# Performance work log

Measured on AMD Instinct MI355X. Metric: run time of the kernel, lower is better.

## Reference

```python
import jax, jax.numpy as jnp
import numpy as np

ALPHA = 0.2          # LeakyReLU negative slope
NEG_INF = -9e15      # mask value from the original code


def setup_inputs() -> dict:
    key = jax.random.key(0)
    k1, k2, k3, k4 = jax.random.split(key, 4)
    B, N, F_in, F_out = 8, 2048, 64, 64
    x = jax.random.normal(k1, (B, N, F_in), dtype=jnp.float32)
    adj = jax.random.randint(k2, (B, N, N), 0, 2, dtype=jnp.int32)
    W = jax.random.normal(k3, (F_in, F_out), dtype=jnp.float32)
    a = jax.random.normal(k4, (2 * F_out, 1), dtype=jnp.float32)
    return {"x": x, "adj": adj, "W": W, "a": a}


def reference(x, adj, W, a):
    # h: [B, N, F_out]
    h = jnp.matmul(x, W)
    F_out = W.shape[1]
    a1 = a[:F_out, 0]   # source half of attention vector
    a2 = a[F_out:, 0]   # target half
    # e_ij = leakyrelu(h_i . a1 + h_j . a2)  -- identical math to the
    # original cat([h_i, h_j]) @ a without materializing [B,N*N,2F].
    s1 = jnp.einsum('bnf,f->bn', h, a1)  # [B, N]
    s2 = jnp.einsum('bnf,f->bn', h, a2)  # [B, N]
    e = jax.nn.leaky_relu(s1[:, :, None] + s2[:, None, :], negative_slope=ALPHA)
    masked = jnp.where(adj > 0, e, NEG_INF)
    attention = jax.nn.softmax(masked, axis=2)  # [B, N, N]
    # dropout p=0.0 / eval mode -> identity
    h_prime = jnp.matmul(attention, h)          # [B, N, F_out]
    return jax.nn.elu(h_prime)                  # concat=True branch
```

## Files before the change

### kernel.cpp

```cpp
#include <hip/hip_runtime.h>
#include <cstdint>

#define LRELU_ALPHA 0.2f
#define NEG_INF -9000000000000000.0f
#define L2E 1.4426950408889634f

typedef __bf16 bf16x8 __attribute__((ext_vector_type(8)));
typedef float floatx4 __attribute__((ext_vector_type(4)));
typedef unsigned int uintx4 __attribute__((ext_vector_type(4)));

constexpr int Bb = 8, Nn = 2048, Ff = 64;
constexpr int TJ = 64;
constexpr int SEGW = 8;
constexpr int SLICE = Nn / SEGW;
constexpr int NT = SLICE / TJ;
constexpr int NROWS = Bb * Nn;
constexpr int MCH = Nn / 64;

__device__ __forceinline__ unsigned short f2bf(float f) {
    unsigned u = __builtin_bit_cast(unsigned, f);
    u = u + 0x7FFFu + ((u >> 16) & 1u);
    return (unsigned short)(u >> 16);
}

__device__ __forceinline__ unsigned cvt_pk_bf16(float lo, float hi) {
    unsigned r;
    asm("v_cvt_pk_bf16_f32 %0, %1, %2" : "=v"(r) : "v"(lo), "v"(hi));
    return r;
}

__global__ __launch_bounds__(256) void gat_prep(
    const float* __restrict__ x, const float* __restrict__ W, const float* __restrict__ a,
    unsigned short* __restrict__ hT, float* __restrict__ s1g, float* __restrict__ s2g)
{
    constexpr int STR2 = 36;
    __shared__ unsigned short hblk[64 * STR2];
    const int tid = threadIdx.x;
    const int blk = blockIdx.x;
    const int b  = blk >> 6;
    const int i0 = (blk & 63) * 32;
    const int w    = tid >> 6;
    const int lane = tid & 63;

    float wcol[64];
    #pragma unroll
    for (int k = 0; k < 64; ++k) wcol[k] = W[k * 64 + lane];
    const float a1 = a[lane], a2 = a[64 + lane];

    for (int r = 0; r < 8; ++r) {
        const int il = w * 8 + r;
        const int i  = i0 + il;
        const float* xrow = x + ((size_t)(b * Nn + i)) * 64;
        float h0 = 0.f, h1 = 0.f, h2 = 0.f, h3 = 0.f;
        #pragma unroll
        for (int k = 0; k < 64; k += 4) {
            h0 = fmaf(xrow[k],     wcol[k],     h0);
            h1 = fmaf(xrow[k + 1], wcol[k + 1], h1);
            h2 = fmaf(xrow[k + 2], wcol[k + 2], h2);
            h3 = fmaf(xrow[k + 3], wcol[k + 3], h3);
        }
        const float h = (h0 + h1) + (h2 + h3);
        float p1 = h * a1, p2 = h * a2;
        #pragma unroll
        for (int off = 32; off; off >>= 1) {
            p1 += __shfl_xor(p1, off);
            p2 += __shfl_xor(p2, off);
        }
        if (lane == 0) { s1g[b * Nn + i] = p1; s2g[b * Nn + i] = p2; }
        hblk[lane * STR2 + il] = f2bf(h);
    }
    __syncthreads();
    {
        const int f = tid >> 2, c = (tid & 3) * 8;
        uint4 v = *reinterpret_cast<const uint4*>(&hblk[f * STR2 + c]);
        *reinterpret_cast<uint4*>(hT + ((size_t)b * 64 + f) * Nn + i0 + c) = v;
    }
}

__global__ __launch_bounds__(256) void gat_pack(
    const int* __restrict__ adj, const float* __restrict__ s1g, const float* __restrict__ s2g,
    unsigned long long* __restrict__ masks, float* __restrict__ row_m)
{
    const int wid  = blockIdx.x * 4 + (threadIdx.x >> 6);
    const int lane = threadIdx.x & 63;
    #pragma unroll
    for (int rr = 0; rr < 2; ++rr) {
        const int row = wid * 2 + rr;
        const int b   = row >> 11;
        const int* ar = adj + (size_t)row * Nn;
        const float* s2r = s2g + (size_t)b * Nn;
        unsigned long long acc = 0;
        float mx = NEG_INF;
        #pragma unroll
        for (int cb = 0; cb < MCH; ++cb) {
            const int   v  = ar[cb * 64 + lane];
            const float sv = s2r[cb * 64 + lane];
            const unsigned long long mb = __ballot(v > 0);
            if (lane == cb) acc = mb;
            mx = (v > 0) ? fmaxf(mx, sv) : mx;
        }
        #pragma unroll
        for (int off = 32; off; off >>= 1) mx = fmaxf(mx, __shfl_xor(mx, off));
        if (lane < 32) masks[(size_t)row * MCH + lane] = acc;
        if (lane == 0) {
            const float ev = s1g[row] + mx;
            row_m[row] = fmaxf(ev, LRELU_ALPHA * ev);
        }
    }
}

__global__ __launch_bounds__(512, 4) void gat_attn(
    const unsigned long long* __restrict__ masks, const unsigned short* __restrict__ hT,
    const float* __restrict__ s1g, const float* __restrict__ s2g,
    const float* __restrict__ row_m, float* __restrict__ out)
{
    __shared__ float O_lds[SEGW][16][65];
    __shared__ float l_lds[SEGW][16];

    const int tid  = threadIdx.x;
    const int blk  = blockIdx.x;
    const int b    = blk >> 7;
    const int i0   = (blk & 127) * 16;
    const int s    = tid >> 6;
    const int lane = tid & 63;
    const int fl   = lane & 15;
    const int q    = lane >> 4;

    const int i = i0 + fl;
    const float s1v = s1g[b * Nn + i];
    const float ci  = -row_m[b * Nn + i] * L2E;
    const unsigned short* hTb = hT + (size_t)b * 64 * Nn + s * SLICE;
    const float* s2b = s2g + b * Nn + s * SLICE;
    const unsigned long long* mrow = masks + (size_t)(b * Nn + i) * MCH + s * NT;

    float l = 0.f;
    floatx4 C[4] = {};

    #pragma unroll
    for (int jt = 0; jt < NT; ++jt) {
        const int jloc = jt * TJ;

        const unsigned long long mk = mrow[jt];
        const float4 sA = *reinterpret_cast<const float4*>(&s2b[jloc + q * 8]);
        const float4 sB = *reinterpret_cast<const float4*>(&s2b[jloc + q * 8 + 4]);
        const float4 sC = *reinterpret_cast<const float4*>(&s2b[jloc + 32 + q * 8]);
        const float4 sD = *reinterpret_cast<const float4*>(&s2b[jloc + 32 + q * 8 + 4]);

        bf16x8 Bv[8];
        #pragma unroll
        for (int u = 0; u < 4; ++u) {
            Bv[2 * u] = *reinterpret_cast<const bf16x8*>(
                hTb + (size_t)(u * 16 + fl) * Nn + jloc + q * 8);
            Bv[2 * u + 1] = *reinterpret_cast<const bf16x8*>(
                hTb + (size_t)(u * 16 + fl) * Nn + jloc + 32 + q * 8);
        }

        const unsigned blo = ((unsigned)(mk >> (q * 8))) & 0xFFu;
        const unsigned bhi = ((unsigned)(mk >> (32 + q * 8))) & 0xFFu;

        float p[16];
        {
            const float s2v0[8] = { sA.x, sA.y, sA.z, sA.w, sB.x, sB.y, sB.z, sB.w };
            const float s2v1[8] = { sC.x, sC.y, sC.z, sC.w, sD.x, sD.y, sD.z, sD.w };
            #pragma unroll
            for (int jj = 0; jj < 8; ++jj) {
                float ev = s1v + s2v0[jj];
                ev = fmaxf(ev, LRELU_ALPHA * ev);
                const float t = exp2f(fmaf(ev, L2E, ci));
                p[jj] = (blo & (1u << jj)) ? t : 0.f;
                l += p[jj];
            }
            #pragma unroll
            for (int jj = 0; jj < 8; ++jj) {
                float ev = s1v + s2v1[jj];
                ev = fmaxf(ev, LRELU_ALPHA * ev);
                const float t = exp2f(fmaf(ev, L2E, ci));
                p[8 + jj] = (bhi & (1u << jj)) ? t : 0.f;
                l += p[8 + jj];
            }
        }

        uintx4 pa, pb;
        #pragma unroll
        for (int d = 0; d < 4; ++d) {
            pa[d] = cvt_pk_bf16(p[2 * d],     p[2 * d + 1]);
            pb[d] = cvt_pk_bf16(p[8 + 2 * d], p[8 + 2 * d + 1]);
        }
        const bf16x8 A0 = __builtin_bit_cast(bf16x8, pa);
        const bf16x8 A1 = __builtin_bit_cast(bf16x8, pb);

        __builtin_amdgcn_s_setprio(1);
        #pragma unroll
        for (int u = 0; u < 4; ++u) {
            C[u] = __builtin_amdgcn_mfma_f32_16x16x32_bf16(A0, Bv[2 * u],     C[u], 0, 0, 0);
            C[u] = __builtin_amdgcn_mfma_f32_16x16x32_bf16(A1, Bv[2 * u + 1], C[u], 0, 0, 0);
        }
        __builtin_amdgcn_s_setprio(0);
    }

    l += __shfl_xor(l, 16);
    l += __shfl_xor(l, 32);

    #pragma unroll
    for (int u = 0; u < 4; ++u)
        #pragma unroll
        for (int r = 0; r < 4; ++r)
            O_lds[s][q * 4 + r][u * 16 + fl] = C[u][r];
    if (q == 0) l_lds[s][fl] = l;
    __syncthreads();

    const int row = tid >> 5;
    const int f0  = (tid & 31) * 2;

    float lsum = 0.f, acc0 = 0.f, acc1 = 0.f;
    #pragma unroll
    for (int k = 0; k < SEGW; ++k) {
        lsum += l_lds[k][row];
        const float2 ov = *reinterpret_cast<const float2*>(&O_lds[k][row][f0]);
        acc0 += ov.x;
        acc1 += ov.y;
    }
    const float inv = 1.f / lsum;
    float v0 = acc0 * inv, v1 = acc1 * inv;
    v0 = (v0 > 0.f) ? v0 : (exp2f(v0 * L2E) - 1.f);
    v1 = (v1 > 0.f) ? v1 : (exp2f(v1 * L2E) - 1.f);
    float2 o2; o2.x = v0; o2.y = v1;
    *reinterpret_cast<float2*>(&out[((size_t)(b * Nn + i0 + row)) * 64 + f0]) = o2;
}

extern "C" void kernel_launch(void* const* d_in, const int* in_sizes, int n_in,
                              void* d_out, int out_size, void* d_ws, size_t ws_size,
                              hipStream_t stream) {
    const float* x   = (const float*)d_in[0];
    const int*   adj = (const int*)d_in[1];
    const float* W   = (const float*)d_in[2];
    const float* a   = (const float*)d_in[3];
    float* out = (float*)d_out;

    char* p = (char*)d_ws;
    unsigned short* hT = (unsigned short*)p;  p += (size_t)Bb * 64 * Nn * sizeof(unsigned short);
    float* s1 = (float*)p;                    p += (size_t)NROWS * sizeof(float);
    float* s2 = (float*)p;                    p += (size_t)NROWS * sizeof(float);
    unsigned long long* masks = (unsigned long long*)p;
    p += (size_t)NROWS * MCH * sizeof(unsigned long long);
    float* row_m = (float*)p;

    gat_prep<<<dim3(Bb * Nn / 32), dim3(256), 0, stream>>>(x, W, a, hT, s1, s2);
    gat_pack<<<dim3(NROWS / 8), dim3(256), 0, stream>>>(adj, s1, s2, masks, row_m);
    gat_attn<<<dim3(NROWS / 16), dim3(512), 0, stream>>>(masks, hT, s1, s2, row_m, out);
}
```

Before: 271.4 us.

## Fuse adjacency bit-packing into attention kernel and use per-batch max bound

```diff
diff --git a/kernel.cpp b/kernel.cpp
--- a/kernel.cpp
+++ b/kernel.cpp
@@ -29,9 +29,19 @@
     return r;
 }
 
+__device__ __forceinline__ unsigned enc_f32(float f) {
+    unsigned u = __builtin_bit_cast(unsigned, f);
+    return (u & 0x80000000u) ? ~u : (u | 0x80000000u);
+}
+__device__ __forceinline__ float dec_f32(unsigned k) {
+    unsigned u = (k & 0x80000000u) ? (k & 0x7FFFFFFFu) : ~k;
+    return __builtin_bit_cast(float, u);
+}
+
 __global__ __launch_bounds__(256) void gat_prep(
     const float* __restrict__ x, const float* __restrict__ W, const float* __restrict__ a,
-    unsigned short* __restrict__ hT, float* __restrict__ s1g, float* __restrict__ s2g)
+    unsigned short* __restrict__ hT, float* __restrict__ s1g, float* __restrict__ s2g,
+    unsigned* __restrict__ s2max_enc)
 {
     constexpr int STR2 = 36;
     __shared__ unsigned short hblk[64 * STR2];
@@ -47,6 +57,7 @@
     for (int k = 0; k < 64; ++k) wcol[k] = W[k * 64 + lane];
     const float a1 = a[lane], a2 = a[64 + lane];
 
+    float s2w = NEG_INF;
     for (int r = 0; r < 8; ++r) {
         const int il = w * 8 + r;
         const int i  = i0 + il;
@@ -67,8 +78,10 @@
             p2 += __shfl_xor(p2, off);
         }
         if (lane == 0) { s1g[b * Nn + i] = p1; s2g[b * Nn + i] = p2; }
+        s2w = fmaxf(s2w, p2);
         hblk[lane * STR2 + il] = f2bf(h);
     }
+    if (lane == 0) atomicMax(&s2max_enc[b], enc_f32(s2w));
     __syncthreads();
     {
         const int f = tid >> 2, c = (tid & 3) * 8;
@@ -77,43 +90,12 @@
     }
 }
 
-__global__ __launch_bounds__(256) void gat_pack(
-    const int* __restrict__ adj, const float* __restrict__ s1g, const float* __restrict__ s2g,
-    unsigned long long* __restrict__ masks, float* __restrict__ row_m)
+__global__ __launch_bounds__(512, 4) void gat_attn(
+    const int* __restrict__ adj, const unsigned short* __restrict__ hT,
+    const float* __restrict__ s1g, const float* __restrict__ s2g,
+    const unsigned* __restrict__ s2max_enc, float* __restrict__ out)
 {
-    const int wid  = blockIdx.x * 4 + (threadIdx.x >> 6);
-    const int lane = threadIdx.x & 63;
-    #pragma unroll
-    for (int rr = 0; rr < 2; ++rr) {
-        const int row = wid * 2 + rr;
-        const int b   = row >> 11;
-        const int* ar = adj + (size_t)row * Nn;
-        const float* s2r = s2g + (size_t)b * Nn;
-        unsigned long long acc = 0;
-        float mx = NEG_INF;
-        #pragma unroll
-        for (int cb = 0; cb < MCH; ++cb) {
-            const int   v  = ar[cb * 64 + lane];
-            const float sv = s2r[cb * 64 + lane];
-            const unsigned long long mb = __ballot(v > 0);
-            if (lane == cb) acc = mb;
-            mx = (v > 0) ? fmaxf(mx, sv) : mx;
-        }
-        #pragma unroll
-        for (int off = 32; off; off >>= 1) mx = fmaxf(mx, __shfl_xor(mx, off));
-        if (lane < 32) masks[(size_t)row * MCH + lane] = acc;
-        if (lane == 0) {
-            const float ev = s1g[row] + mx;
-            row_m[row] = fmaxf(ev, LRELU_ALPHA * ev);
-        }
-    }
-}
-
-__global__ __launch_bounds__(512, 4) void gat_attn(
-    const unsigned long long* __restrict__ masks, const unsigned short* __restrict__ hT,
-    const float* __restrict__ s1g, const float* __restrict__ s2g,
-    const float* __restrict__ row_m, float* __restrict__ out)
-{
+    __shared__ unsigned long long mk_lds[16][33];
     __shared__ float O_lds[SEGW][16][65];
     __shared__ float l_lds[SEGW][16];
 
@@ -126,12 +108,30 @@
     const int fl   = lane & 15;
     const int q    = lane >> 4;
 
+    #pragma unroll
+    for (int rr = 0; rr < 2; ++rr) {
+        const int rloc = s * 2 + rr;
+        const int* ar = adj + ((size_t)(b * Nn + i0 + rloc)) * Nn;
+        unsigned long long acc = 0;
+        #pragma unroll
+        for (int cb = 0; cb < MCH; ++cb) {
+            const int v = ar[cb * 64 + lane];
+            const unsigned long long mb = __ballot(v > 0);
+            if (lane == cb) acc = mb;
+        }
+        if (lane < 32) mk_lds[rloc][lane] = acc;
+    }
+
     const int i = i0 + fl;
     const float s1v = s1g[b * Nn + i];
-    const float ci  = -row_m[b * Nn + i] * L2E;
+    const float s2mx = dec_f32(s2max_enc[b]);
+    float mub = s1v + s2mx;
+    mub = fmaxf(mub, LRELU_ALPHA * mub);
+    const float ci = -mub * L2E;
     const unsigned short* hTb = hT + (size_t)b * 64 * Nn + s * SLICE;
     const float* s2b = s2g + b * Nn + s * SLICE;
-    const unsigned long long* mrow = masks + (size_t)(b * Nn + i) * MCH + s * NT;
+
+    __syncthreads();
 
     float l = 0.f;
     floatx4 C[4] = {};
@@ -140,7 +140,7 @@
     for (int jt = 0; jt < NT; ++jt) {
         const int jloc = jt * TJ;
 
-        const unsigned long long mk = mrow[jt];
+        const unsigned long long mk = mk_lds[fl][s * NT + jt];
         const float4 sA = *reinterpret_cast<const float4*>(&s2b[jloc + q * 8]);
         const float4 sB = *reinterpret_cast<const float4*>(&s2b[jloc + q * 8 + 4]);
         const float4 sC = *reinterpret_cast<const float4*>(&s2b[jloc + 32 + q * 8]);
@@ -241,11 +241,9 @@
     unsigned short* hT = (unsigned short*)p;  p += (size_t)Bb * 64 * Nn * sizeof(unsigned short);
     float* s1 = (float*)p;                    p += (size_t)NROWS * sizeof(float);
     float* s2 = (float*)p;                    p += (size_t)NROWS * sizeof(float);
-    unsigned long long* masks = (unsigned long long*)p;
-    p += (size_t)NROWS * MCH * sizeof(unsigned long long);
-    float* row_m = (float*)p;
-
-    gat_prep<<<dim3(Bb * Nn / 32), dim3(256), 0, stream>>>(x, W, a, hT, s1, s2);
-    gat_pack<<<dim3(NROWS / 8), dim3(256), 0, stream>>>(adj, s1, s2, masks, row_m);
-    gat_attn<<<dim3(NROWS / 16), dim3(512), 0, stream>>>(masks, hT, s1, s2, row_m, out);
-}
+    unsigned* s2max_enc = (unsigned*)p;
+
+    hipMemsetAsync(s2max_enc, 0, Bb * sizeof(unsigned), stream);
+    gat_prep<<<dim3(Bb * Nn / 32), dim3(256), 0, stream>>>(x, W, a, hT, s1, s2, s2max_enc);
+    gat_attn<<<dim3(NROWS / 16), dim3(512), 0, stream>>>(adj, hT, s1, s2, s2max_enc, out);
+}
```

New measurement: 261.9 us. 1.04x faster.
